# Performance work log

Hardware: AMD Instinct MI355X
Metric: run time of the kernel (lower is better)

Reference implementation:

```python
import jax, jax.numpy as jnp
import numpy as np

WINDOW = 1024
HOP = 256

def setup_inputs() -> dict:
    key = jax.random.key(0)
    X = jax.random.normal(key, (16, 2, 262144), dtype=jnp.float32)
    return {"X": X}

def reference(X):
    # X: (B, 2, T) with channel 0 = Re, channel 1 = Im.
    # Identity-weight Conv1d(1, window, kernel=window, stride=hop) is exactly
    # strided framing: frame t is X[..., t*hop : t*hop + window].
    B, _, T = X.shape
    n_frames = (T - WINDOW) // HOP + 1
    # (n_frames, WINDOW) gather index into the time axis
    idx = jnp.arange(n_frames)[:, None] * HOP + jnp.arange(WINDOW)[None, :]
    frames = X[:, :, idx]                      # (B, 2, n_frames, WINDOW)
    return jnp.transpose(frames, (0, 1, 3, 2)) # (B, 2, WINDOW, n_frames)
```

## Files before the change

kernel.cpp:

```cpp
#include <hip/hip_runtime.h>

#define WINDOW_SZ 1024
#define HOP_SZ    256
#define NFRAMES   1021
#define T_LEN     262144

#define WROWS 16
#define REGION (WROWS * NFRAMES)
#define NPASS_LD 8
#define NVEC4 (REGION / 4)

typedef float f4 __attribute__((ext_vector_type(4)));

__global__ __launch_bounds__(512)
void frame_transpose_kernel(const float* __restrict__ X,
                            float* __restrict__ out) {
    __shared__ float lds[REGION];

    const int bid  = blockIdx.x;
    const int work = ((bid & 7) << 8) | (bid >> 3);
    const int bc    = work >> 6;
    const int wt    = work & 63;
    const int outer = wt >> 2;
    const int inner = wt & 3;
    const int w0    = inner * 256 + outer * 16;

    const int tid = threadIdx.x;
    const float* Xbc = X + (size_t)bc * T_LEN;

    {
        const int q  = tid & 3;
        const int fo = tid >> 2;
        const int wl = 4 * q;
#pragma unroll
        for (int p = 0; p < NPASS_LD; ++p) {
            const int f = p * 128 + fo;
            if (f < NFRAMES) {
                const f4 v = *(const f4*)(Xbc + (size_t)f * HOP_SZ + w0 + wl);
                lds[(wl + 0) * NFRAMES + f] = v.x;
                lds[(wl + 1) * NFRAMES + f] = v.y;
                lds[(wl + 2) * NFRAMES + f] = v.z;
                lds[(wl + 3) * NFRAMES + f] = v.w;
            }
        }
    }

    __syncthreads();

    {
        float* obase = out + (size_t)(bc * WINDOW_SZ + w0) * NFRAMES;
#pragma unroll
        for (int p = 0; p < 8; ++p) {
            const int idx = p * 512 + tid;
            if (idx < NVEC4) {
                const f4 t = *(const f4*)&lds[4 * idx];
                *(f4*)(obase + 4 * (size_t)idx) = t;
            }
        }
    }
}

extern "C" void kernel_launch(void* const* d_in, const int* in_sizes, int n_in,
                              void* d_out, int out_size, void* d_ws, size_t ws_size,
                              hipStream_t stream) {
    const float* X = (const float*)d_in[0];
    float* out = (float*)d_out;

    dim3 block(512, 1, 1);
    dim3 grid(32 * 64, 1, 1);
    frame_transpose_kernel<<<grid, block, 0, stream>>>(X, out);
}
```

Before: 173.1 us.

## Load each hop-line once and emit four window offsets per block

Exploits the overlap between frames: out[w][f] = X[f*256+w], so the rows w, w+256, w+512 and w+768 come from the same 256-strided lines shifted by one frame. Each block now loads 1024 lines × 16 columns once into LDS and writes the four output row groups by shifting within LDS. This cuts global reads by four and reduces the grid from 2048 to 512 blocks. The cost is unaligned vector stores, shuffle work per output, and fewer, longer-running blocks, which may lower occupancy or hurt store coalescing.

```diff
diff --git a/kernel.cpp b/kernel.cpp
--- a/kernel.cpp
+++ b/kernel.cpp
@@ -5,56 +5,58 @@
 #define NFRAMES   1021
 #define T_LEN     262144
 
-#define WROWS 16
-#define REGION (WROWS * NFRAMES)
-#define NPASS_LD 8
-#define NVEC4 (REGION / 4)
+#define NLINES 1024
+#define WG_ROWS 16
 
-typedef float f4 __attribute__((ext_vector_type(4)));
+typedef float f4  __attribute__((ext_vector_type(4)));
+typedef float f4u __attribute__((ext_vector_type(4), aligned(4)));
 
 __global__ __launch_bounds__(512)
 void frame_transpose_kernel(const float* __restrict__ X,
                             float* __restrict__ out) {
-    __shared__ float lds[REGION];
+    __shared__ float lds[WG_ROWS * NLINES];
 
-    const int bid  = blockIdx.x;
-    const int work = ((bid & 7) << 8) | (bid >> 3);
-    const int bc    = work >> 6;
-    const int wt    = work & 63;
-    const int outer = wt >> 2;
-    const int inner = wt & 3;
-    const int w0    = inner * 256 + outer * 16;
+    const int bid = blockIdx.x;
+    const int bc  = bid >> 4;
+    const int wg  = bid & 15;
+    const int t   = threadIdx.x;
 
-    const int tid = threadIdx.x;
-    const float* Xbc = X + (size_t)bc * T_LEN;
+    const float* Xbc = X + (size_t)bc * T_LEN + wg * 16;
 
-    {
-        const int q  = tid & 3;
-        const int fo = tid >> 2;
-        const int wl = 4 * q;
 #pragma unroll
-        for (int p = 0; p < NPASS_LD; ++p) {
-            const int f = p * 128 + fo;
-            if (f < NFRAMES) {
-                const f4 v = *(const f4*)(Xbc + (size_t)f * HOP_SZ + w0 + wl);
-                lds[(wl + 0) * NFRAMES + f] = v.x;
-                lds[(wl + 1) * NFRAMES + f] = v.y;
-                lds[(wl + 2) * NFRAMES + f] = v.z;
-                lds[(wl + 3) * NFRAMES + f] = v.w;
-            }
-        }
+    for (int p = 0; p < 8; ++p) {
+        const int idx  = p * 512 + t;
+        const int line = idx >> 2;
+        const int sub  = idx & 3;
+        const f4 v = *(const f4*)(Xbc + line * HOP_SZ + 4 * sub);
+        lds[(4 * sub + 0) * NLINES + line] = v.x;
+        lds[(4 * sub + 1) * NLINES + line] = v.y;
+        lds[(4 * sub + 2) * NLINES + line] = v.z;
+        lds[(4 * sub + 3) * NLINES + line] = v.w;
     }
 
     __syncthreads();
 
-    {
-        float* obase = out + (size_t)(bc * WINDOW_SZ + w0) * NFRAMES;
+#pragma unroll
+    for (int k = 0; k < 4; ++k) {
+        float* obase = out + (size_t)(bc * WINDOW_SZ + 256 * k + 16 * wg) * NFRAMES;
 #pragma unroll
         for (int p = 0; p < 8; ++p) {
-            const int idx = p * 512 + tid;
-            if (idx < NVEC4) {
-                const f4 t = *(const f4*)&lds[4 * idx];
-                *(f4*)(obase + 4 * (size_t)idx) = t;
+            const int slot = p * 512 + t;
+            const int row  = slot >> 8;
+            const int pos  = slot & 255;
+            const float* lrow = &lds[row * NLINES + 4 * pos];
+            if (pos < 255) {
+                const f4 q0 = *(const f4*)(lrow);
+                const f4 q1 = *(const f4*)(lrow + 4);
+                f4 o;
+                if      (k == 0) o = q0;
+                else if (k == 1) o = f4{q0.y, q0.z, q0.w, q1.x};
+                else if (k == 2) o = f4{q0.z, q0.w, q1.x, q1.y};
+                else             o = f4{q0.w, q1.x, q1.y, q1.z};
+                *(f4u*)(obase + (size_t)row * NFRAMES + 4 * pos) = o;
+            } else {
+                obase[(size_t)row * NFRAMES + 1020] = lrow[k];
             }
         }
     }
@@ -67,6 +69,6 @@
     float* out = (float*)d_out;
 
     dim3 block(512, 1, 1);
-    dim3 grid(32 * 64, 1, 1);
+    dim3 grid(32 * 16, 1, 1);
     frame_transpose_kernel<<<grid, block, 0, stream>>>(X, out);
 }
```

New measurement: 157.4 us. 9.1% less time.
